# Kernel optimization log

Hardware: AMD Instinct MI355X
Metric: run time of the kernel (lower is better)

## Reference

```python
import jax, jax.numpy as jnp
import numpy as np

N = 20000
E = 320000
F_IN = 512
F_OUT = 512
DIFF_T = 1.0
NUM_STEPS = 5
TIME_DECAY = 0.1
LN_EPS = 1e-5


def setup_inputs() -> dict:
    key = jax.random.key(0)
    k_x, k_e, k_ts, k_wt, k_wr = jax.random.split(key, 5)
    x = jax.random.normal(k_x, (N, F_IN), dtype=jnp.float32)
    edge_index = jax.random.randint(k_e, (2, E), 0, N)
    timestamps = jax.random.uniform(k_ts, (E,), dtype=jnp.float32) * 100.0
    lim = float(np.sqrt(6.0 / (F_IN + F_OUT)))  # xavier_uniform
    W_t = jax.random.uniform(k_wt, (F_OUT, F_IN), jnp.float32, -lim, lim)
    b_t = jnp.zeros((F_OUT,), jnp.float32)
    W_r = jax.random.uniform(k_wr, (F_OUT, F_IN), jnp.float32, -lim, lim)
    gamma = jnp.ones((F_OUT,), jnp.float32)
    beta = jnp.zeros((F_OUT,), jnp.float32)
    return {"node_features": x, "edge_index": edge_index, "timestamps": timestamps,
            "W_t": W_t, "b_t": b_t, "W_r": W_r, "gamma": gamma, "beta": beta,
            "graph_time": 100}


def reference(node_features, edge_index, timestamps, W_t, b_t, W_r, gamma, beta, graph_time):
    x = node_features
    n = x.shape[0]
    # append self-loops with timestamp == graph.time
    loop = jnp.arange(n)
    ei = jnp.concatenate([edge_index, jnp.stack([loop, loop], axis=0)], axis=1)
    ts = jnp.concatenate([timestamps, jnp.full((n,), graph_time, jnp.float32)])
    src, dst = ei[0], ei[1]
    # time-decayed symmetric-normalized adjacency weights
    w = jnp.exp(-TIME_DECAY * (ts.max() - ts))  # [E+N]
    deg = jax.ops.segment_sum(w, dst, num_segments=n)  # [N]
    dinv = jnp.where(deg > 0, deg ** -0.5, 0.0)
    ew = dinv[src] * w * dinv[dst]  # [E+N]
    # K Euler steps of heat diffusion: h <- h + dt*(A_norm h - h)
    dt = DIFF_T / NUM_STEPS
    h = x
    for _ in range(NUM_STEPS):
        diffused = jax.ops.segment_sum(ew[:, None] * h[src], dst, num_segments=n)  # [N, F]
        h = h + dt * (diffused - h)
    # transform + residual + layernorm (dropout omitted: eval mode)
    out = jax.nn.relu(h @ W_t.T + b_t) + x @ W_r.T  # [N, F_OUT]
    mu = out.mean(axis=-1, keepdims=True)
    var = out.var(axis=-1, keepdims=True)
    out = (out - mu) * jax.lax.rsqrt(var + LN_EPS) * gamma + beta
    return out
```

## Files before the change

### kernel.cpp

```cpp
#include <hip/hip_runtime.h>
#include <hip/hip_fp16.h>

#define FDIM 512
#define TDK  0.1f
#define DTs  0.2f
#define EPSv 1e-5f

using bf16x8  = __attribute__((ext_vector_type(8))) __bf16;
using floatx4 = __attribute__((ext_vector_type(4))) float;
using ushort8 = __attribute__((ext_vector_type(8))) unsigned short;
using uintx4  = __attribute__((ext_vector_type(4))) unsigned int;

__device__ __forceinline__ unsigned short f2bf(float f) {
  unsigned int u = __float_as_uint(f);
  u += 0x7fffu + ((u >> 16) & 1u);
  return (unsigned short)(u >> 16);
}

__device__ __forceinline__ void gld16(const __bf16* g, __bf16* l) {
  __builtin_amdgcn_global_load_lds(
      (const __attribute__((address_space(1))) unsigned int*)g,
      (__attribute__((address_space(3))) unsigned int*)l, 16, 0, 0);
}

__global__ __launch_bounds__(256) void edge_w_deg(const int* __restrict__ src, const int* __restrict__ dst,
                                                  const float* __restrict__ ts, const int* __restrict__ gt_p,
                                                  float* __restrict__ w, unsigned long long* __restrict__ pc,
                                                  int E, int N) {
  int e = blockIdx.x * blockDim.x + threadIdx.x;
  int total = E + N;
  if (e >= total) return;
  float gtf = (float)(*gt_p);
  int d; float t;
  if (e < E) { d = dst[e]; t = ts[e]; }
  else       { d = e - E;  t = gtf; }
  float wv = expf(TDK * (t - gtf));
  w[e] = wv;
  unsigned long long pk = (1ULL << 52) + (unsigned long long)(wv * 4294967296.0f);
  atomicAdd(&pc[d], pk);
}

__global__ __launch_bounds__(256) void seg_reduce(const unsigned long long* __restrict__ pc,
                                                  int* __restrict__ bsum, int n) {
  int i = blockIdx.x * 256 + threadIdx.x;
  int v = (i < n) ? (((int)(pc[i] >> 52) + 3) & ~3) : 0;
  for (int o = 32; o; o >>= 1) v += __shfl_down(v, o);
  __shared__ int sm[4];
  if ((threadIdx.x & 63) == 0) sm[threadIdx.x >> 6] = v;
  __syncthreads();
  if (threadIdx.x == 0) bsum[blockIdx.x] = sm[0] + sm[1] + sm[2] + sm[3];
}

__global__ __launch_bounds__(256) void scan_bsum(const int* __restrict__ bsum, int* __restrict__ bbase,
                                                 int* __restrict__ offsN, int nb) {
  __shared__ int sm[256];
  int t = threadIdx.x;
  int v = (t < nb) ? bsum[t] : 0;
  sm[t] = v;
  __syncthreads();
  for (int o = 1; o < 256; o <<= 1) {
    int u = (t >= o) ? sm[t - o] : 0;
    __syncthreads();
    sm[t] += u;
    __syncthreads();
  }
  if (t < nb) bbase[t] = sm[t] - v;
  if (t == nb - 1) offsN[0] = sm[t];
}

__global__ __launch_bounds__(256) void seg_scan(const unsigned long long* __restrict__ pc,
                                                const int* __restrict__ bbase,
                                                int* __restrict__ offs, int* __restrict__ cursor,
                                                float* __restrict__ dinv, int n) {
  __shared__ int sm[256];
  int i = blockIdx.x * 256 + threadIdx.x;
  unsigned long long p = (i < n) ? pc[i] : 0ULL;
  int v = ((int)(p >> 52) + 3) & ~3;
  sm[threadIdx.x] = v;
  __syncthreads();
  for (int o = 1; o < 256; o <<= 1) {
    int u = (threadIdx.x >= o) ? sm[threadIdx.x - o] : 0;
    __syncthreads();
    sm[threadIdx.x] += u;
    __syncthreads();
  }
  int excl = sm[threadIdx.x] - v + bbase[blockIdx.x];
  if (i < n) {
    offs[i] = excl; cursor[i] = excl;
    float deg = (float)(p & ((1ULL << 52) - 1ULL)) * (1.0f / 4294967296.0f);
    dinv[i] = (deg > 0.f) ? rsqrtf(deg) : 0.f;
  }
}

__global__ __launch_bounds__(256) void scatter_kernel(const int* __restrict__ src, const int* __restrict__ dst,
                                                      const float* __restrict__ w, const float* __restrict__ dinv,
                                                      int* __restrict__ cursor, unsigned* __restrict__ cv,
                                                      int E, int N) {
  int e = blockIdx.x * blockDim.x + threadIdx.x;
  if (e >= E + N) return;
  int s, d;
  if (e < E) { s = src[e]; d = dst[e]; }
  else       { s = d = e - E; }
  int pos = atomicAdd(&cursor[d], 1);
  float v = dinv[s] * w[e] * dinv[d];
  unsigned short hv = __half_as_ushort(__float2half(v));
  cv[pos] = (unsigned)s | ((unsigned)hv << 16);
}

__device__ __forceinline__ void acc8(uintx4 u, float v, float* a) {
  a[0] += v * __uint_as_float(u[0] << 16);
  a[1] += v * __uint_as_float(u[0] & 0xffff0000u);
  a[2] += v * __uint_as_float(u[1] << 16);
  a[3] += v * __uint_as_float(u[1] & 0xffff0000u);
  a[4] += v * __uint_as_float(u[2] << 16);
  a[5] += v * __uint_as_float(u[2] & 0xffff0000u);
  a[6] += v * __uint_as_float(u[3] << 16);
  a[7] += v * __uint_as_float(u[3] & 0xffff0000u);
}

__device__ __forceinline__ float cvval(unsigned cu) {
  return __half2float(__ushort_as_half((unsigned short)(cu >> 16)));
}

__global__ __launch_bounds__(256) void spmm_xcd(const int* __restrict__ offs, const unsigned* __restrict__ cv,
                                                const unsigned short* __restrict__ h_in,
                                                unsigned short* __restrict__ h_out, int N) {
  int chunk = blockIdx.x & 7;
  int tile  = blockIdx.x >> 3;
  int row = tile * 32 + (threadIdx.x >> 3);
  if (row >= N) return;
  int fo = chunk * 64 + (threadIdx.x & 7) * 8;
  const unsigned short* hp = h_in + fo;
  int s = offs[row], e = offs[row + 1];
  float a[8] = {0.f, 0.f, 0.f, 0.f, 0.f, 0.f, 0.f, 0.f};
  int j = s;
  for (; j + 8 <= e; j += 8) {
    unsigned cu[8]; uintx4 u[8];
#pragma unroll
    for (int t = 0; t < 8; ++t) cu[t] = cv[j + t];
#pragma unroll
    for (int t = 0; t < 8; ++t) u[t] = *(const uintx4*)(hp + ((cu[t] & 0xffffu) << 9));
#pragma unroll
    for (int t = 0; t < 8; ++t) acc8(u[t], cvval(cu[t]), a);
  }
  if (j < e) {
    unsigned cu[4]; uintx4 u[4];
#pragma unroll
    for (int t = 0; t < 4; ++t) cu[t] = cv[j + t];
#pragma unroll
    for (int t = 0; t < 4; ++t) u[t] = *(const uintx4*)(hp + ((cu[t] & 0xffffu) << 9));
#pragma unroll
    for (int t = 0; t < 4; ++t) acc8(u[t], cvval(cu[t]), a);
  }
  uintx4 ud = *(const uintx4*)(hp + (row << 9));
  float hd[8];
  hd[0] = __uint_as_float(ud[0] << 16); hd[1] = __uint_as_float(ud[0] & 0xffff0000u);
  hd[2] = __uint_as_float(ud[1] << 16); hd[3] = __uint_as_float(ud[1] & 0xffff0000u);
  hd[4] = __uint_as_float(ud[2] << 16); hd[5] = __uint_as_float(ud[2] & 0xffff0000u);
  hd[6] = __uint_as_float(ud[3] << 16); hd[7] = __uint_as_float(ud[3] & 0xffff0000u);
  uintx4 o;
  unsigned int p0, p1;
#define PACK(k0, k1, dst_)                                        \
  { float o0 = hd[k0] + DTs * (a[k0] - hd[k0]);                   \
    float o1 = hd[k1] + DTs * (a[k1] - hd[k1]);                   \
    p0 = f2bf(o0); p1 = f2bf(o1); dst_ = p0 | (p1 << 16); }
  PACK(0, 1, o[0]) PACK(2, 3, o[1]) PACK(4, 5, o[2]) PACK(6, 7, o[3])
#undef PACK
  __builtin_nontemporal_store(o, (uintx4*)(h_out + (size_t)row * FDIM + fo));
}

__global__ __launch_bounds__(256) void cast_all(const float* __restrict__ x, const float* __restrict__ wt,
                                                const float* __restrict__ wr,
                                                unsigned short* __restrict__ xb, unsigned short* __restrict__ wtb,
                                                unsigned short* __restrict__ wrb, int n8x, int n8w) {
  int i = blockIdx.x * blockDim.x + threadIdx.x;
  const float* sp; unsigned short* dp; int k;
  if (i < n8x)                { sp = x;  dp = xb;  k = i; }
  else if (i < n8x + n8w)     { sp = wt; dp = wtb; k = i - n8x; }
  else if (i < n8x + 2 * n8w) { sp = wr; dp = wrb; k = i - n8x - n8w; }
  else return;
  const float4 v0 = *(const float4*)(sp + (size_t)k * 8);
  const float4 v1 = *(const float4*)(sp + (size_t)k * 8 + 4);
  ushort8 o;
  o[0] = f2bf(v0.x); o[1] = f2bf(v0.y); o[2] = f2bf(v0.z); o[3] = f2bf(v0.w);
  o[4] = f2bf(v1.x); o[5] = f2bf(v1.y); o[6] = f2bf(v1.z); o[7] = f2bf(v1.w);
  *(ushort8*)(dp + (size_t)k * 8) = o;
}

__global__ __launch_bounds__(256, 3) void gemm_fused(const __bf16* __restrict__ Ah, const __bf16* __restrict__ Ax,
                                                     const __bf16* __restrict__ Wt, const __bf16* __restrict__ Wr,
                                                     const float* __restrict__ bias, float* __restrict__ out,
                                                     int M, int NB) {
  __shared__ __bf16 sA[2][128 * 32];
  __shared__ __bf16 sB[2][128 * 32];
  int tid = threadIdx.x;
  int wid = tid >> 6, lane = tid & 63;
  int wm = wid & 1, wn = wid >> 1;
  int lane15 = lane & 15, quad = lane >> 4;

  int d = blockIdx.x;
  int x = d & 7, s = d >> 3;
  int q = NB >> 3, r = NB & 7;
  int g = (x < r ? x * (q + 1) : r * (q + 1) + (x - r) * q) + s;
  int mi = g >> 2, ni = g & 3;
  int m0 = mi * 128, n0 = ni * 128;

  int r0 = wid * 32 + (lane >> 2);
  int c0 = ((((lane & 3) - (lane >> 3)) & 3)) * 8;
  int am0 = m0 + r0;      if (am0 >= M) am0 = M - 1;
  int am1 = m0 + r0 + 16; if (am1 >= M) am1 = M - 1;
  int bn0 = n0 + r0;
  const __bf16* a00 = Ah + (size_t)am0 * FDIM + c0;
  const __bf16* a01 = Ah + (size_t)am1 * FDIM + c0;
  const __bf16* a10 = Ax + (size_t)am0 * FDIM + c0;
  const __bf16* a11 = Ax + (size_t)am1 * FDIM + c0;
  const __bf16* b00 = Wt + (size_t)bn0 * FDIM + c0;
  const __bf16* b01 = Wt + (size_t)(bn0 + 16) * FDIM + c0;
  const __bf16* b10 = Wr + (size_t)bn0 * FDIM + c0;
  const __bf16* b11 = Wr + (size_t)(bn0 + 16) * FDIM + c0;
  int loff0 = wid * 1024;
  int loff1 = wid * 1024 + 512;

  auto stage = [&](int b, const __bf16* pa0, const __bf16* pa1,
                   const __bf16* pb0, const __bf16* pb1, int kt) {
    gld16(pa0 + kt, &sA[b][loff0]); gld16(pa1 + kt, &sA[b][loff1]);
    gld16(pb0 + kt, &sB[b][loff0]); gld16(pb1 + kt, &sB[b][loff1]);
  };

  int koff = ((quad + (lane15 >> 1)) & 3) * 8;

  float bn[4];
#pragma unroll
  for (int in = 0; in < 4; ++in) bn[in] = bias[n0 + wn * 64 + in * 16 + lane15];

  floatx4 acc[4][4];
  floatx4 z4; z4[0] = 0.f; z4[1] = 0.f; z4[2] = 0.f; z4[3] = 0.f;
#pragma unroll
  for (int im = 0; im < 4; ++im)
#pragma unroll
    for (int in = 0; in < 4; ++in) acc[im][in] = z4;

  stage(0, a00, a01, b00, b01, 0);
  for (int it = 0; it < 32; ++it) {
    int cb = it & 1;
    __syncthreads();
    int nx = it + 1;
    if (nx < 32) {
      if (nx < 16) stage(1 - cb, a00, a01, b00, b01, nx * 32);
      else         stage(1 - cb, a10, a11, b10, b11, (nx & 15) * 32);
    }
    if (it == 16) {
#pragma unroll
      for (int im = 0; im < 4; ++im)
#pragma unroll
        for (int in = 0; in < 4; ++in)
#pragma unroll
          for (int rr = 0; rr < 4; ++rr)
            acc[im][in][rr] = fmaxf(acc[im][in][rr] + bn[in], 0.f);
    }
    bf16x8 af[4], br[4];
#pragma unroll
    for (int im = 0; im < 4; ++im)
      af[im] = *(const bf16x8*)(&sA[cb][(wm * 64 + im * 16 + lane15) * 32 + koff]);
#pragma unroll
    for (int in = 0; in < 4; ++in)
      br[in] = *(const bf16x8*)(&sB[cb][(wn * 64 + in * 16 + lane15) * 32 + koff]);
#pragma unroll
    for (int im = 0; im < 4; ++im)
#pragma unroll
      for (int in = 0; in < 4; ++in)
        acc[im][in] = __builtin_amdgcn_mfma_f32_16x16x32_bf16(af[im], br[in], acc[im][in], 0, 0, 0);
  }

#pragma unroll
  for (int im = 0; im < 4; ++im) {
#pragma unroll
    for (int in = 0; in < 4; ++in) {
#pragma unroll
      for (int rr = 0; rr < 4; ++rr) {
        int m = m0 + wm * 64 + im * 16 + quad * 4 + rr;
        int n = n0 + wn * 64 + in * 16 + lane15;
        if (m < M) out[(size_t)m * FDIM + n] = acc[im][in][rr];
      }
    }
  }
}

__global__ __launch_bounds__(256) void ln_kernel(const float* __restrict__ pre, const float* __restrict__ gamma,
                                                 const float* __restrict__ beta, float* __restrict__ out) {
  int row = blockIdx.x, t = threadIdx.x;
  float2 v = *(const float2*)(pre + (size_t)row * FDIM + t * 2);
  float s = v.x + v.y;
  float ss = v.x * v.x + v.y * v.y;
  for (int off = 32; off; off >>= 1) { s += __shfl_down(s, off); ss += __shfl_down(ss, off); }
  __shared__ float sm[4], sm2[4];
  int wid = t >> 6, lane = t & 63;
  if (lane == 0) { sm[wid] = s; sm2[wid] = ss; }
  __syncthreads();
  if (t == 0) {
    float a = sm[0] + sm[1] + sm[2] + sm[3];
    float b = sm2[0] + sm2[1] + sm2[2] + sm2[3];
    sm[0] = a; sm2[0] = b;
  }
  __syncthreads();
  float mu = sm[0] * (1.f / FDIM);
  float var = sm2[0] * (1.f / FDIM) - mu * mu;
  float inv = rsqrtf(var + EPSv);
  float2 g  = *(const float2*)(gamma + t * 2);
  float2 bb = *(const float2*)(beta + t * 2);
  float2 o;
  o.x = (v.x - mu) * inv * g.x + bb.x;
  o.y = (v.y - mu) * inv * g.y + bb.y;
  *(float2*)(out + (size_t)row * FDIM + t * 2) = o;
}

extern "C" void kernel_launch(void* const* d_in, const int* in_sizes, int n_in,
                              void* d_out, int out_size, void* d_ws, size_t ws_size,
                              hipStream_t stream) {
  const float* x     = (const float*)d_in[0];
  const int*   ei    = (const int*)d_in[1];
  const float* ts    = (const float*)d_in[2];
  const float* W_t   = (const float*)d_in[3];
  const float* b_t   = (const float*)d_in[4];
  const float* W_r   = (const float*)d_in[5];
  const float* gamma = (const float*)d_in[6];
  const float* beta  = (const float*)d_in[7];
  const int*   gt    = (const int*)d_in[8];

  const int E = in_sizes[2];
  const int N = in_sizes[0] / FDIM;
  const int* src = ei;
  const int* dst = ei + E;
  const int totE = E + N;
  const int totEp = totE + 3 * N;
  const int nb = (N + 255) / 256;

  char* base = (char*)d_ws;
  size_t off = 0;
  auto carve = [&](size_t bytes) -> char* {
    char* r = base + off;
    off = (off + bytes + 255) & ~(size_t)255;
    return r;
  };
  unsigned long long* pc = (unsigned long long*)carve((size_t)N * 8);
  unsigned* cv = (unsigned*)carve((size_t)totEp * 4);
  size_t zero_bytes = off;
  float* dinv  = (float*)carve((size_t)N * 4);
  int*   offs  = (int*)  carve((size_t)(N + 1) * 4);
  int*   cursor= (int*)  carve((size_t)N * 4);
  int*   bsum  = (int*)  carve((size_t)nb * 4);
  int*   bbase = (int*)  carve((size_t)nb * 4);
  float* w     = (float*)carve((size_t)totE * 4);
  unsigned short* xb  = (unsigned short*)carve((size_t)N * FDIM * 2);
  unsigned short* hba = (unsigned short*)carve((size_t)N * FDIM * 2);
  unsigned short* hbb = (unsigned short*)carve((size_t)N * FDIM * 2);
  unsigned short* wtb = (unsigned short*)carve((size_t)FDIM * FDIM * 2);
  unsigned short* wrb = (unsigned short*)carve((size_t)FDIM * FDIM * 2);
  float* preLN = (float*)carve((size_t)N * FDIM * 4);

  hipMemsetAsync(d_ws, 0, zero_bytes, stream);

  edge_w_deg<<<(totE + 255) / 256, 256, 0, stream>>>(src, dst, ts, gt, w, pc, E, N);
  seg_reduce<<<nb, 256, 0, stream>>>(pc, bsum, N);
  scan_bsum<<<1, 256, 0, stream>>>(bsum, bbase, offs + N, nb);
  seg_scan<<<nb, 256, 0, stream>>>(pc, bbase, offs, cursor, dinv, N);
  scatter_kernel<<<(totE + 255) / 256, 256, 0, stream>>>(src, dst, w, dinv, cursor, cv, E, N);

  int n8x = N * FDIM / 8;
  int n8w = FDIM * FDIM / 8;
  int n8tot = n8x + 2 * n8w;
  cast_all<<<(n8tot + 255) / 256, 256, 0, stream>>>(x, W_t, W_r, xb, wtb, wrb, n8x, n8w);

  int sgrid = ((N + 31) / 32) * 8;
  spmm_xcd<<<sgrid, 256, 0, stream>>>(offs, cv, xb,  hba, N);
  spmm_xcd<<<sgrid, 256, 0, stream>>>(offs, cv, hba, hbb, N);
  spmm_xcd<<<sgrid, 256, 0, stream>>>(offs, cv, hbb, hba, N);
  spmm_xcd<<<sgrid, 256, 0, stream>>>(offs, cv, hba, hbb, N);
  spmm_xcd<<<sgrid, 256, 0, stream>>>(offs, cv, hbb, hba, N);

  int MB = (N + 127) / 128;
  int NBLK = MB * (FDIM / 128);
  gemm_fused<<<NBLK, 256, 0, stream>>>((const __bf16*)hba, (const __bf16*)xb,
                                       (const __bf16*)wtb, (const __bf16*)wrb,
                                       b_t, preLN, N, NBLK);

  ln_kernel<<<N, 256, 0, stream>>>(preLN, gamma, beta, (float*)d_out);
}
```

Measured before the change: 353.8 us.

## Fuse graph preprocessing and casts, use decoupled lookback scan and atomic-returned positions

Merges edge weight/degree computation with the bf16 casts into one grid-stride kernel, replaces the three-kernel segmented scan with a single-pass lookback scan, and derives each edge's CSR slot from the old value returned by the degree atomic, so the second atomic pass in scatter goes away. This cuts kernel launches and one round of atomics on the cursor array. The lookback spins on per-block aggregates, which relies on earlier blocks being scheduled; it only works with nb small enough to be co-resident. It also assumes per-node in-degree fits in 16 bits.

```diff
diff --git a/kernel.cpp b/kernel.cpp
--- a/kernel.cpp
+++ b/kernel.cpp
@@ -23,39 +23,52 @@
       (__attribute__((address_space(3))) unsigned int*)l, 16, 0, 0);
 }
 
-__global__ __launch_bounds__(256) void edge_w_deg(const int* __restrict__ src, const int* __restrict__ dst,
-                                                  const float* __restrict__ ts, const int* __restrict__ gt_p,
-                                                  float* __restrict__ w, unsigned long long* __restrict__ pc,
-                                                  int E, int N) {
-  int e = blockIdx.x * blockDim.x + threadIdx.x;
-  int total = E + N;
-  if (e >= total) return;
+__global__ __launch_bounds__(256) void prep_kernel(
+    const int* __restrict__ src, const int* __restrict__ dst,
+    const float* __restrict__ ts, const int* __restrict__ gt_p,
+    const float* __restrict__ x, const float* __restrict__ W_t, const float* __restrict__ W_r,
+    float* __restrict__ w, unsigned short* __restrict__ pos16,
+    unsigned long long* __restrict__ pc,
+    unsigned short* __restrict__ xb, unsigned short* __restrict__ wtb, unsigned short* __restrict__ wrb,
+    int E, int N, int n8x, int n8w) {
+  int tid = blockIdx.x * blockDim.x + threadIdx.x;
+  int stride = gridDim.x * blockDim.x;
+  int totE = E + N;
   float gtf = (float)(*gt_p);
-  int d; float t;
-  if (e < E) { d = dst[e]; t = ts[e]; }
-  else       { d = e - E;  t = gtf; }
-  float wv = expf(TDK * (t - gtf));
-  w[e] = wv;
-  unsigned long long pk = (1ULL << 52) + (unsigned long long)(wv * 4294967296.0f);
-  atomicAdd(&pc[d], pk);
-}
-
-__global__ __launch_bounds__(256) void seg_reduce(const unsigned long long* __restrict__ pc,
-                                                  int* __restrict__ bsum, int n) {
-  int i = blockIdx.x * 256 + threadIdx.x;
-  int v = (i < n) ? (((int)(pc[i] >> 52) + 3) & ~3) : 0;
-  for (int o = 32; o; o >>= 1) v += __shfl_down(v, o);
-  __shared__ int sm[4];
-  if ((threadIdx.x & 63) == 0) sm[threadIdx.x >> 6] = v;
-  __syncthreads();
-  if (threadIdx.x == 0) bsum[blockIdx.x] = sm[0] + sm[1] + sm[2] + sm[3];
-}
-
-__global__ __launch_bounds__(256) void scan_bsum(const int* __restrict__ bsum, int* __restrict__ bbase,
-                                                 int* __restrict__ offsN, int nb) {
+  for (int e = tid; e < totE; e += stride) {
+    int d; float t;
+    if (e < E) { d = dst[e]; t = ts[e]; }
+    else       { d = e - E;  t = gtf; }
+    float wv = expf(TDK * (t - gtf));
+    w[e] = wv;
+    unsigned long long pk = (1ULL << 52) + (unsigned long long)(wv * 4294967296.0f);
+    unsigned long long old = atomicAdd(&pc[d], pk);
+    pos16[e] = (unsigned short)(old >> 52);
+  }
+  int n8tot = n8x + 2 * n8w;
+  for (int i = tid; i < n8tot; i += stride) {
+    const float* sp; unsigned short* dp; int k;
+    if (i < n8x)            { sp = x;   dp = xb;  k = i; }
+    else if (i < n8x + n8w) { sp = W_t; dp = wtb; k = i - n8x; }
+    else                    { sp = W_r; dp = wrb; k = i - n8x - n8w; }
+    const float4 v0 = *(const float4*)(sp + (size_t)k * 8);
+    const float4 v1 = *(const float4*)(sp + (size_t)k * 8 + 4);
+    ushort8 o;
+    o[0] = f2bf(v0.x); o[1] = f2bf(v0.y); o[2] = f2bf(v0.z); o[3] = f2bf(v0.w);
+    o[4] = f2bf(v1.x); o[5] = f2bf(v1.y); o[6] = f2bf(v1.z); o[7] = f2bf(v1.w);
+    *(ushort8*)(dp + (size_t)k * 8) = o;
+  }
+}
+
+__global__ __launch_bounds__(256) void scan_lookback(
+    const unsigned long long* __restrict__ pc, int* __restrict__ agg,
+    int* __restrict__ offs, float* __restrict__ dinv, int N, int nb) {
   __shared__ int sm[256];
-  int t = threadIdx.x;
-  int v = (t < nb) ? bsum[t] : 0;
+  __shared__ int wsum[4];
+  int b = blockIdx.x, t = threadIdx.x;
+  int i = b * 256 + t;
+  unsigned long long p = (i < N) ? pc[i] : 0ULL;
+  int v = ((int)(p >> 52) + 3) & ~3;
   sm[t] = v;
   __syncthreads();
   for (int o = 1; o < 256; o <<= 1) {
@@ -64,44 +77,37 @@
     sm[t] += u;
     __syncthreads();
   }
-  if (t < nb) bbase[t] = sm[t] - v;
-  if (t == nb - 1) offsN[0] = sm[t];
-}
-
-__global__ __launch_bounds__(256) void seg_scan(const unsigned long long* __restrict__ pc,
-                                                const int* __restrict__ bbase,
-                                                int* __restrict__ offs, int* __restrict__ cursor,
-                                                float* __restrict__ dinv, int n) {
-  __shared__ int sm[256];
-  int i = blockIdx.x * 256 + threadIdx.x;
-  unsigned long long p = (i < n) ? pc[i] : 0ULL;
-  int v = ((int)(p >> 52) + 3) & ~3;
-  sm[threadIdx.x] = v;
+  int total = sm[255];
+  if (t == 0) atomicExch(&agg[b], total);
+  int part = 0;
+  for (int k = t; k < b; k += 256) {
+    int a;
+    do { a = atomicAdd(&agg[k], 0); } while (a == 0);
+    part += a;
+  }
+  for (int o = 32; o; o >>= 1) part += __shfl_down(part, o);
+  if ((t & 63) == 0) wsum[t >> 6] = part;
   __syncthreads();
-  for (int o = 1; o < 256; o <<= 1) {
-    int u = (threadIdx.x >= o) ? sm[threadIdx.x - o] : 0;
-    __syncthreads();
-    sm[threadIdx.x] += u;
-    __syncthreads();
-  }
-  int excl = sm[threadIdx.x] - v + bbase[blockIdx.x];
-  if (i < n) {
-    offs[i] = excl; cursor[i] = excl;
+  int base = wsum[0] + wsum[1] + wsum[2] + wsum[3];
+  int excl = base + sm[t] - v;
+  if (i < N) {
+    offs[i] = excl;
     float deg = (float)(p & ((1ULL << 52) - 1ULL)) * (1.0f / 4294967296.0f);
     dinv[i] = (deg > 0.f) ? rsqrtf(deg) : 0.f;
   }
+  if (b == nb - 1 && t == 255) offs[N] = base + total;
 }
 
 __global__ __launch_bounds__(256) void scatter_kernel(const int* __restrict__ src, const int* __restrict__ dst,
-                                                      const float* __restrict__ w, const float* __restrict__ dinv,
-                                                      int* __restrict__ cursor, unsigned* __restrict__ cv,
-                                                      int E, int N) {
+                                                      const float* __restrict__ w, const unsigned short* __restrict__ pos16,
+                                                      const float* __restrict__ dinv, const int* __restrict__ offs,
+                                                      unsigned* __restrict__ cv, int E, int N) {
   int e = blockIdx.x * blockDim.x + threadIdx.x;
   if (e >= E + N) return;
   int s, d;
   if (e < E) { s = src[e]; d = dst[e]; }
   else       { s = d = e - E; }
-  int pos = atomicAdd(&cursor[d], 1);
+  int pos = offs[d] + (int)pos16[e];
   float v = dinv[s] * w[e] * dinv[d];
   unsigned short hv = __half_as_ushort(__float2half(v));
   cv[pos] = (unsigned)s | ((unsigned)hv << 16);
@@ -169,24 +175,6 @@
   __builtin_nontemporal_store(o, (uintx4*)(h_out + (size_t)row * FDIM + fo));
 }
 
-__global__ __launch_bounds__(256) void cast_all(const float* __restrict__ x, const float* __restrict__ wt,
-                                                const float* __restrict__ wr,
-                                                unsigned short* __restrict__ xb, unsigned short* __restrict__ wtb,
-                                                unsigned short* __restrict__ wrb, int n8x, int n8w) {
-  int i = blockIdx.x * blockDim.x + threadIdx.x;
-  const float* sp; unsigned short* dp; int k;
-  if (i < n8x)                { sp = x;  dp = xb;  k = i; }
-  else if (i < n8x + n8w)     { sp = wt; dp = wtb; k = i - n8x; }
-  else if (i < n8x + 2 * n8w) { sp = wr; dp = wrb; k = i - n8x - n8w; }
-  else return;
-  const float4 v0 = *(const float4*)(sp + (size_t)k * 8);
-  const float4 v1 = *(const float4*)(sp + (size_t)k * 8 + 4);
-  ushort8 o;
-  o[0] = f2bf(v0.x); o[1] = f2bf(v0.y); o[2] = f2bf(v0.z); o[3] = f2bf(v0.w);
-  o[4] = f2bf(v1.x); o[5] = f2bf(v1.y); o[6] = f2bf(v1.z); o[7] = f2bf(v1.w);
-  *(ushort8*)(dp + (size_t)k * 8) = o;
-}
-
 __global__ __launch_bounds__(256, 3) void gemm_fused(const __bf16* __restrict__ Ah, const __bf16* __restrict__ Ax,
                                                      const __bf16* __restrict__ Wt, const __bf16* __restrict__ Wr,
                                                      const float* __restrict__ bias, float* __restrict__ out,
@@ -344,13 +332,12 @@
   };
   unsigned long long* pc = (unsigned long long*)carve((size_t)N * 8);
   unsigned* cv = (unsigned*)carve((size_t)totEp * 4);
+  int* agg     = (int*)carve((size_t)nb * 4);
   size_t zero_bytes = off;
   float* dinv  = (float*)carve((size_t)N * 4);
   int*   offs  = (int*)  carve((size_t)(N + 1) * 4);
-  int*   cursor= (int*)  carve((size_t)N * 4);
-  int*   bsum  = (int*)  carve((size_t)nb * 4);
-  int*   bbase = (int*)  carve((size_t)nb * 4);
   float* w     = (float*)carve((size_t)totE * 4);
+  unsigned short* pos16 = (unsigned short*)carve((size_t)totE * 2);
   unsigned short* xb  = (unsigned short*)carve((size_t)N * FDIM * 2);
   unsigned short* hba = (unsigned short*)carve((size_t)N * FDIM * 2);
   unsigned short* hbb = (unsigned short*)carve((size_t)N * FDIM * 2);
@@ -360,16 +347,13 @@
 
   hipMemsetAsync(d_ws, 0, zero_bytes, stream);
 
-  edge_w_deg<<<(totE + 255) / 256, 256, 0, stream>>>(src, dst, ts, gt, w, pc, E, N);
-  seg_reduce<<<nb, 256, 0, stream>>>(pc, bsum, N);
-  scan_bsum<<<1, 256, 0, stream>>>(bsum, bbase, offs + N, nb);
-  seg_scan<<<nb, 256, 0, stream>>>(pc, bbase, offs, cursor, dinv, N);
-  scatter_kernel<<<(totE + 255) / 256, 256, 0, stream>>>(src, dst, w, dinv, cursor, cv, E, N);
-
   int n8x = N * FDIM / 8;
   int n8w = FDIM * FDIM / 8;
-  int n8tot = n8x + 2 * n8w;
-  cast_all<<<(n8tot + 255) / 256, 256, 0, stream>>>(x, W_t, W_r, xb, wtb, wrb, n8x, n8w);
+
+  prep_kernel<<<2048, 256, 0, stream>>>(src, dst, ts, gt, x, W_t, W_r,
+                                        w, pos16, pc, xb, wtb, wrb, E, N, n8x, n8w);
+  scan_lookback<<<nb, 256, 0, stream>>>(pc, agg, offs, dinv, N, nb);
+  scatter_kernel<<<(totE + 255) / 256, 256, 0, stream>>>(src, dst, w, pos16, dinv, offs, cv, E, N);
 
   int sgrid = ((N + 31) / 32) * 8;
   spmm_xcd<<<sgrid, 256, 0, stream>>>(offs, cv, xb,  hba, N);
```

Result: faster. 339.5 us (-4.1%).
